# Kernel optimization log

Hardware: AMD Instinct MI355X
Metric: run time of the kernel (lower is better)

The kernel has to match this reference:

```python
import jax, jax.numpy as jnp
import numpy as np

H = 12        # num heads
DH = 64       # head dim
W = 8         # window size
WIN2 = W * W  # tokens per window


def _relative_position_index():
    # Swin-style relative position index, [WIN2, WIN2] int array (static).
    coords = np.stack(np.meshgrid(np.arange(W), np.arange(W), indexing='ij'))  # [2,W,W]
    flat = coords.reshape(2, -1)                                               # [2,WIN2]
    rel = flat[:, :, None] - flat[:, None, :]                                  # [2,WIN2,WIN2]
    rel = rel.transpose(1, 2, 0).astype(np.int64)
    rel[..., 0] += W - 1
    rel[..., 1] += W - 1
    rel[..., 0] *= 2 * W - 1
    return rel.sum(-1)  # [WIN2, WIN2]


def setup_inputs() -> dict:
    key = jax.random.key(0)
    ks = jax.random.split(key, 12)
    B, S, D = 128, 256, 768
    scale = 0.02
    return {
        'q': jax.random.normal(ks[0], (B, S, D), jnp.float32),
        'k': jax.random.normal(ks[1], (B, S, D), jnp.float32),
        'v': jax.random.normal(ks[2], (B, S, D), jnp.float32),
        'Wq': jax.random.normal(ks[3], (D, D), jnp.float32) * scale,
        'bq': jnp.zeros((D,), jnp.float32),
        'Wk': jax.random.normal(ks[4], (D, D), jnp.float32) * scale,
        'bk': jnp.zeros((D,), jnp.float32),
        'Wv': jax.random.normal(ks[5], (D, D), jnp.float32) * scale,
        'bv': jnp.zeros((D,), jnp.float32),
        'Wo': jax.random.normal(ks[6], (D, D), jnp.float32) * scale,
        'bo': jnp.zeros((D,), jnp.float32),
        'bias_table': jax.random.normal(ks[7], ((2 * W - 1) ** 2, H), jnp.float32) * scale,
    }


def reference(q, k, v, Wq, bq, Wk, bk, Wv, bv, Wo, bo, bias_table):
    B, S, D = q.shape

    def proj(x, Wt, bt):
        # Linear stores weight as [out, in]; y = x @ W^T + b, then split heads.
        return (x @ Wt.T + bt).reshape(B, S, H, DH).transpose(0, 2, 1, 3)

    qh = proj(q, Wq, bq)  # [B,H,S,DH]
    kh = proj(k, Wk, bk)
    vh = proj(v, Wv, bv)

    scores = jnp.einsum('bhqd,bhkd->bhqk', qh, kh) / np.float32(np.sqrt(DH))

    idx = _relative_position_index()                         # static [WIN2,WIN2]
    bias = bias_table[idx.reshape(-1)].reshape(WIN2, WIN2, H)
    bias = bias.transpose(2, 0, 1)                           # [H,WIN2,WIN2]
    n_contrast = S // WIN2
    bias = jnp.tile(bias, (1, n_contrast, n_contrast))       # [H,S,S]

    probs = jax.nn.softmax(scores + bias[None], axis=-1)     # dropout p=0 (eval)
    ctx = jnp.einsum('bhqk,bhkd->bhqd', probs, vh)
    ctx = ctx.transpose(0, 2, 1, 3).reshape(B, S, D)
    return ctx @ Wo.T + bo
```

## Files before the change

kernel.cpp:

```cpp
#include <hip/hip_runtime.h>


typedef __bf16 bf16;
typedef __bf16 bf16x8 __attribute__((ext_vector_type(8)));
typedef float  f32x4  __attribute__((ext_vector_type(4)));

#define MFMA_BF16(a, b, c) __builtin_amdgcn_mfma_f32_16x16x32_bf16((a), (b), (c), 0, 0, 0)

__device__ __forceinline__ void gld16(const void* g, void* l) {
    __builtin_amdgcn_global_load_lds(
        (const __attribute__((address_space(1))) void*)g,
        (__attribute__((address_space(3))) void*)l, 16, 0, 0);
}

__device__ __forceinline__ bf16x8 pack8(f32x4 lo, f32x4 hi) {
    bf16x8 r;
    r[0] = (bf16)lo[0]; r[1] = (bf16)lo[1]; r[2] = (bf16)lo[2]; r[3] = (bf16)lo[3];
    r[4] = (bf16)hi[0]; r[5] = (bf16)hi[1]; r[6] = (bf16)hi[2]; r[7] = (bf16)hi[3];
    return r;
}

__device__ __forceinline__ int swz8(int row, int g) { return g ^ (row & 7); }

__global__ __launch_bounds__(256)
void gemm_qkv(const float* __restrict__ q, const float* __restrict__ k,
              const float* __restrict__ v,
              const float* __restrict__ Wq, const float* __restrict__ Wk,
              const float* __restrict__ Wv,
              const float* __restrict__ bq, const float* __restrict__ bk,
              const float* __restrict__ bv, bf16* __restrict__ outbase)
{
    __shared__ bf16 As[128 * 64];
    __shared__ bf16 Bs[128 * 64];

    const int z = blockIdx.z;
    const float* X    = (z == 0) ? q  : (z == 1) ? k  : v;
    const float* Wt   = (z == 0) ? Wq : (z == 1) ? Wk : Wv;
    const float* bias = (z == 0) ? bq : (z == 1) ? bk : bv;
    bf16* out = outbase + (size_t)z * 25165824;

    const int tid  = threadIdx.x;
    const int m0   = blockIdx.x * 128;
    const int n0   = blockIdx.y * 128;
    const int w    = tid >> 6;
    const int lane = tid & 63;
    const int quad = lane >> 4;
    const int l15  = lane & 15;
    const int wr   = (w >> 1) * 64;
    const int wc   = (w & 1) * 64;

    f32x4 acc[4][4] = {};

    for (int kt = 0; kt < 12; ++kt) {
        const int k0 = kt * 64;
        __syncthreads();
        #pragma unroll
        for (int p = 0; p < 4; ++p) {
            int g = p * 256 + tid;
            int row = g >> 3, gp = g & 7;
            const float* src = X + (size_t)(m0 + row) * 768 + k0 + gp * 8;
            *(bf16x8*)&As[row * 64 + swz8(row, gp) * 8] =
                pack8(*(const f32x4*)src, *(const f32x4*)(src + 4));
        }
        #pragma unroll
        for (int p = 0; p < 4; ++p) {
            int g = p * 256 + tid;
            int row = g >> 3, gp = g & 7;
            const float* src = Wt + (size_t)(n0 + row) * 768 + k0 + gp * 8;
            *(bf16x8*)&Bs[row * 64 + swz8(row, gp) * 8] =
                pack8(*(const f32x4*)src, *(const f32x4*)(src + 4));
        }
        __syncthreads();
        #pragma unroll
        for (int kk = 0; kk < 2; ++kk) {
            bf16x8 af[4], bfr[4];
            #pragma unroll
            for (int mt = 0; mt < 4; ++mt) {
                int row = wr + mt * 16 + l15;
                af[mt] = *(const bf16x8*)&As[row * 64 + swz8(row, kk * 4 + quad) * 8];
            }
            #pragma unroll
            for (int nt = 0; nt < 4; ++nt) {
                int row = wc + nt * 16 + l15;
                bfr[nt] = *(const bf16x8*)&Bs[row * 64 + swz8(row, kk * 4 + quad) * 8];
            }
            #pragma unroll
            for (int mt = 0; mt < 4; ++mt)
                #pragma unroll
                for (int nt = 0; nt < 4; ++nt)
                    acc[mt][nt] = MFMA_BF16(af[mt], bfr[nt], acc[mt][nt]);
        }
    }

    #pragma unroll
    for (int mt = 0; mt < 4; ++mt) {
        #pragma unroll
        for (int nt = 0; nt < 4; ++nt) {
            int gn = n0 + wc + nt * 16 + l15;
            float bv = bias[gn];
            int h = gn >> 6, d = gn & 63;
            #pragma unroll
            for (int r = 0; r < 4; ++r) {
                int gm = m0 + wr + mt * 16 + quad * 4 + r;
                int b = gm >> 8, s = gm & 255;
                out[(((size_t)(b * 12 + h) << 8) + s) * 64 + d] = (bf16)(acc[mt][nt][r] + bv);
            }
        }
    }
}

__global__ __launch_bounds__(256)
void gemm_out(const bf16* __restrict__ X, const float* __restrict__ Wt,
              const float* __restrict__ bias, float* __restrict__ out)
{
    __shared__ bf16 As[128 * 64];
    __shared__ bf16 Bs[128 * 64];

    const int tid  = threadIdx.x;
    const int m0   = blockIdx.x * 128;
    const int n0   = blockIdx.y * 128;
    const int w    = tid >> 6;
    const int lane = tid & 63;
    const int quad = lane >> 4;
    const int l15  = lane & 15;
    const int wr   = (w >> 1) * 64;
    const int wc   = (w & 1) * 64;

    f32x4 acc[4][4] = {};

    for (int kt = 0; kt < 12; ++kt) {
        const int k0 = kt * 64;
        __syncthreads();
        #pragma unroll
        for (int p = 0; p < 4; ++p) {
            int g = p * 256 + tid;
            int row = g >> 3;
            int cg  = swz8(row, g & 7);
            gld16(X + (size_t)(m0 + row) * 768 + k0 + cg * 8,
                  (char*)As + g * 16);
        }
        #pragma unroll
        for (int p = 0; p < 4; ++p) {
            int g = p * 256 + tid;
            int row = g >> 3, gp = g & 7;
            const float* src = Wt + (size_t)(n0 + row) * 768 + k0 + gp * 8;
            *(bf16x8*)&Bs[row * 64 + swz8(row, gp) * 8] =
                pack8(*(const f32x4*)src, *(const f32x4*)(src + 4));
        }
        __syncthreads();
        #pragma unroll
        for (int kk = 0; kk < 2; ++kk) {
            bf16x8 af[4], bfr[4];
            #pragma unroll
            for (int mt = 0; mt < 4; ++mt) {
                int row = wr + mt * 16 + l15;
                af[mt] = *(const bf16x8*)&As[row * 64 + swz8(row, kk * 4 + quad) * 8];
            }
            #pragma unroll
            for (int nt = 0; nt < 4; ++nt) {
                int row = wc + nt * 16 + l15;
                bfr[nt] = *(const bf16x8*)&Bs[row * 64 + swz8(row, kk * 4 + quad) * 8];
            }
            #pragma unroll
            for (int mt = 0; mt < 4; ++mt)
                #pragma unroll
                for (int nt = 0; nt < 4; ++nt)
                    acc[mt][nt] = MFMA_BF16(af[mt], bfr[nt], acc[mt][nt]);
        }
    }

    #pragma unroll
    for (int mt = 0; mt < 4; ++mt) {
        #pragma unroll
        for (int nt = 0; nt < 4; ++nt) {
            int gn = n0 + wc + nt * 16 + l15;
            float bv = bias[gn];
            #pragma unroll
            for (int r = 0; r < 4; ++r) {
                int gm = m0 + wr + mt * 16 + quad * 4 + r;
                out[(size_t)gm * 768 + gn] = acc[mt][nt][r] + bv;
            }
        }
    }
}

__global__ __launch_bounds__(256)
void transpose_v(const bf16* __restrict__ vh, bf16* __restrict__ vt)
{
    __shared__ bf16 Ts[64 * 65];
    const int qt = blockIdx.x, h = blockIdx.y, b = blockIdx.z;
    const bf16* src = vh + ((size_t)(b * 12 + h) * 256 + qt * 64) * 64;
    bf16* dst = vt + (size_t)(b * 12 + h) * 64 * 256;

    const int tid = threadIdx.x;
    {
        int row = tid >> 2, c0 = (tid & 3) * 16;
        bf16x8 v0 = *(const bf16x8*)(src + row * 64 + c0);
        bf16x8 v1 = *(const bf16x8*)(src + row * 64 + c0 + 8);
        #pragma unroll
        for (int i = 0; i < 8; ++i) {
            Ts[row * 65 + c0 + i]     = v0[i];
            Ts[row * 65 + c0 + 8 + i] = v1[i];
        }
    }
    __syncthreads();
    {
        int d = tid >> 2, j0 = (tid & 3) * 16;
        bf16x8 o0, o1;
        #pragma unroll
        for (int i = 0; i < 8; ++i) {
            o0[i] = Ts[(j0 + i) * 65 + d];
            o1[i] = Ts[(j0 + 8 + i) * 65 + d];
        }
        *(bf16x8*)(dst + (size_t)d * 256 + qt * 64 + j0)     = o0;
        *(bf16x8*)(dst + (size_t)d * 256 + qt * 64 + j0 + 8) = o1;
    }
}

__global__ __launch_bounds__(256)
void attn_kernel(const bf16* __restrict__ qh, const bf16* __restrict__ kh,
                 const bf16* __restrict__ vt, const float* __restrict__ table,
                 bf16* __restrict__ ctx)
{
    __shared__ bf16 Qs[64 * 64];
    __shared__ bf16 Ks[64 * 64];
    __shared__ bf16 Vs[64 * 64];
    __shared__ bf16 Ps[4 * 16 * 72];
    __shared__ bf16 Bsh[64 * 68];

    const int tid  = threadIdx.x;
    const int qt   = blockIdx.x;
    const int h    = blockIdx.y;
    const int b    = blockIdx.z;
    const int w    = tid >> 6;
    const int lane = tid & 63;
    const int quad = lane >> 4;
    const int l15  = lane & 15;

    const size_t bh = (size_t)(b * 12 + h) * 256 * 64;
    const bf16* Qg  = qh + bh + (size_t)qt * 64 * 64;
    const bf16* Kg  = kh + bh;
    const bf16* Vtg = vt + bh;

    #pragma unroll
    for (int p = 0; p < 2; ++p) {
        int g = p * 256 + tid;
        gld16(Qg + (size_t)(g >> 3) * 64 + (g & 7) * 8, (char*)Qs + g * 16);
    }
    {
        int i = tid >> 2, j0 = (tid & 3) * 16;
        int ai = i >> 3, aj = i & 7;
        #pragma unroll
        for (int jj = 0; jj < 16; ++jj) {
            int j = j0 + jj;
            int idx = (ai - (j >> 3) + 7) * 15 + (aj - (j & 7) + 7);
            Bsh[i * 68 + j] = (bf16)table[idx * 12 + h];
        }
    }

    f32x4 sacc[16] = {};
    bf16x8 qf0, qf1;
    for (int c = 0; c < 4; ++c) {
        __syncthreads();
        #pragma unroll
        for (int p = 0; p < 2; ++p) {
            int g = p * 256 + tid;
            gld16(Kg + (size_t)(c * 64 + (g >> 3)) * 64 + (g & 7) * 8, (char*)Ks + g * 16);
        }
        __syncthreads();
        if (c == 0) {
            qf0 = *(const bf16x8*)&Qs[(w * 16 + l15) * 64 + quad * 8];
            qf1 = *(const bf16x8*)&Qs[(w * 16 + l15) * 64 + 32 + quad * 8];
        }
        #pragma unroll
        for (int jtl = 0; jtl < 4; ++jtl) {
            bf16x8 kf0 = *(const bf16x8*)&Ks[(jtl * 16 + l15) * 64 + quad * 8];
            bf16x8 kf1 = *(const bf16x8*)&Ks[(jtl * 16 + l15) * 64 + 32 + quad * 8];
            sacc[c * 4 + jtl] = MFMA_BF16(qf0, kf0, sacc[c * 4 + jtl]);
            sacc[c * 4 + jtl] = MFMA_BF16(qf1, kf1, sacc[c * 4 + jtl]);
        }
    }

    const int browbase = w * 16 + quad * 4;
    float p[16][4];
    #pragma unroll
    for (int jt = 0; jt < 16; ++jt) {
        int jcol = ((jt * 16) & 63) + l15;
        #pragma unroll
        for (int r = 0; r < 4; ++r)
            p[jt][r] = sacc[jt][r] * 0.125f + (float)Bsh[(browbase + r) * 68 + jcol];
    }
    float invl[4];
    #pragma unroll
    for (int r = 0; r < 4; ++r) {
        float m = p[0][r];
        #pragma unroll
        for (int jt = 1; jt < 16; ++jt) m = fmaxf(m, p[jt][r]);
        #pragma unroll
        for (int off = 1; off < 16; off <<= 1)
            m = fmaxf(m, __shfl_xor(m, off, 64));
        float s = 0.f;
        #pragma unroll
        for (int jt = 0; jt < 16; ++jt) {
            p[jt][r] = __expf(p[jt][r] - m);
            s += p[jt][r];
        }
        #pragma unroll
        for (int off = 1; off < 16; off <<= 1)
            s += __shfl_xor(s, off, 64);
        invl[r] = 1.0f / s;
    }

    f32x4 cacc[4] = {};
    bf16* Pw = &Ps[w * 16 * 72];
    for (int c = 0; c < 4; ++c) {
        __syncthreads();
        #pragma unroll
        for (int pp = 0; pp < 2; ++pp) {
            int g = pp * 256 + tid;
            gld16(Vtg + (size_t)(g >> 3) * 256 + c * 64 + (g & 7) * 8, (char*)Vs + g * 16);
        }
        #pragma unroll
        for (int jtl = 0; jtl < 4; ++jtl) {
            int jt = c * 4 + jtl;
            #pragma unroll
            for (int r = 0; r < 4; ++r)
                Pw[(quad * 4 + r) * 72 + jtl * 16 + l15] = (bf16)(p[jt][r] * invl[r]);
        }
        __syncthreads();
        bf16x8 pf0 = *(const bf16x8*)&Pw[l15 * 72 + quad * 8];
        bf16x8 pf1 = *(const bf16x8*)&Pw[l15 * 72 + 32 + quad * 8];
        #pragma unroll
        for (int dt = 0; dt < 4; ++dt) {
            bf16x8 vf0 = *(const bf16x8*)&Vs[(dt * 16 + l15) * 64 + quad * 8];
            bf16x8 vf1 = *(const bf16x8*)&Vs[(dt * 16 + l15) * 64 + 32 + quad * 8];
            cacc[dt] = MFMA_BF16(pf0, vf0, cacc[dt]);
            cacc[dt] = MFMA_BF16(pf1, vf1, cacc[dt]);
        }
    }

    const size_t obase = ((size_t)b * 256) * 768 + (size_t)h * 64;
    #pragma unroll
    for (int dt = 0; dt < 4; ++dt) {
        #pragma unroll
        for (int r = 0; r < 4; ++r) {
            int s = qt * 64 + w * 16 + quad * 4 + r;
            int d = dt * 16 + l15;
            ctx[obase + (size_t)s * 768 + d] = (bf16)cacc[dt][r];
        }
    }
}

extern "C" void kernel_launch(void* const* d_in, const int* in_sizes, int n_in,
                              void* d_out, int out_size, void* d_ws, size_t ws_size,
                              hipStream_t stream) {
    (void)in_sizes; (void)n_in; (void)out_size; (void)ws_size;
    const float* q     = (const float*)d_in[0];
    const float* k     = (const float*)d_in[1];
    const float* v     = (const float*)d_in[2];
    const float* Wq    = (const float*)d_in[3];
    const float* bq    = (const float*)d_in[4];
    const float* Wk    = (const float*)d_in[5];
    const float* bk    = (const float*)d_in[6];
    const float* Wv    = (const float*)d_in[7];
    const float* bv    = (const float*)d_in[8];
    const float* Wo    = (const float*)d_in[9];
    const float* bo    = (const float*)d_in[10];
    const float* table = (const float*)d_in[11];

    const size_t NE = (size_t)128 * 256 * 768;
    bf16* qh  = (bf16*)d_ws;
    bf16* kh  = qh + NE;
    bf16* vh  = kh + NE;
    bf16* vt  = vh + NE;
    bf16* ctx = vh;
    float* out = (float*)d_out;

    dim3 blk(256);
    gemm_qkv<<<dim3(256, 6, 3), blk, 0, stream>>>(q, k, v, Wq, Wk, Wv, bq, bk, bv, qh);
    transpose_v<<<dim3(4, 12, 128), blk, 0, stream>>>(vh, vt);
    attn_kernel<<<dim3(4, 12, 128), blk, 0, stream>>>(qh, kh, vt, table, ctx);
    gemm_out<<<dim3(256, 6), blk, 0, stream>>>(ctx, Wo, bo, out);
}
```

Measured before the change: 777.9 us.

## Double-buffer LDS tiles with register prefetch in projection GEMMs

Both the QKV projection GEMM and the output projection GEMM now use two LDS buffers. The next K-tile is loaded from global memory into registers while MFMAs run on the current tile, and one barrier per iteration replaces two. The goal is to hide global load latency behind compute. The cost is doubled shared memory (64KB per block), more registers for the prefetched fp32 data, and possibly lower occupancy. In gemm_out the direct global-to-LDS loads are replaced by ordinary register loads.

Result: faster. 739.2 us (-5.0%).

```diff
diff --git a/kernel.cpp b/kernel.cpp
--- a/kernel.cpp
+++ b/kernel.cpp
@@ -30,8 +30,8 @@
               const float* __restrict__ bq, const float* __restrict__ bk,
               const float* __restrict__ bv, bf16* __restrict__ outbase)
 {
-    __shared__ bf16 As[128 * 64];
-    __shared__ bf16 Bs[128 * 64];
+    __shared__ bf16 As[2][128 * 64];
+    __shared__ bf16 Bs[2][128 * 64];
 
     const int z = blockIdx.z;
     const float* X    = (z == 0) ? q  : (z == 1) ? k  : v;
@@ -49,40 +49,49 @@
     const int wr   = (w >> 1) * 64;
     const int wc   = (w & 1) * 64;
 
+    int srow[4], sgp[4], sdst[4];
+    #pragma unroll
+    for (int p = 0; p < 4; ++p) {
+        int g = p * 256 + tid;
+        srow[p] = g >> 3;
+        sgp[p]  = g & 7;
+        sdst[p] = srow[p] * 64 + swz8(srow[p], sgp[p]) * 8;
+    }
+
     f32x4 acc[4][4] = {};
-
-    for (int kt = 0; kt < 12; ++kt) {
-        const int k0 = kt * 64;
-        __syncthreads();
+    f32x4 aL[4], aH[4], bL[4], bH[4];
+
+    auto load_stage = [&](int k0) {
         #pragma unroll
         for (int p = 0; p < 4; ++p) {
-            int g = p * 256 + tid;
-            int row = g >> 3, gp = g & 7;
-            const float* src = X + (size_t)(m0 + row) * 768 + k0 + gp * 8;
-            *(bf16x8*)&As[row * 64 + swz8(row, gp) * 8] =
-                pack8(*(const f32x4*)src, *(const f32x4*)(src + 4));
-        }
+            const float* sa = X + (size_t)(m0 + srow[p]) * 768 + k0 + sgp[p] * 8;
+            aL[p] = *(const f32x4*)sa;
+            aH[p] = *(const f32x4*)(sa + 4);
+            const float* sb = Wt + (size_t)(n0 + srow[p]) * 768 + k0 + sgp[p] * 8;
+            bL[p] = *(const f32x4*)sb;
+            bH[p] = *(const f32x4*)(sb + 4);
+        }
+    };
+    auto write_stage = [&](int buf) {
         #pragma unroll
         for (int p = 0; p < 4; ++p) {
-            int g = p * 256 + tid;
-            int row = g >> 3, gp = g & 7;
-            const float* src = Wt + (size_t)(n0 + row) * 768 + k0 + gp * 8;
-            *(bf16x8*)&Bs[row * 64 + swz8(row, gp) * 8] =
-                pack8(*(const f32x4*)src, *(const f32x4*)(src + 4));
-        }
-        __syncthreads();
+            *(bf16x8*)&As[buf][sdst[p]] = pack8(aL[p], aH[p]);
+            *(bf16x8*)&Bs[buf][sdst[p]] = pack8(bL[p], bH[p]);
+        }
+    };
+    auto compute = [&](int buf) {
         #pragma unroll
         for (int kk = 0; kk < 2; ++kk) {
             bf16x8 af[4], bfr[4];
             #pragma unroll
             for (int mt = 0; mt < 4; ++mt) {
                 int row = wr + mt * 16 + l15;
-                af[mt] = *(const bf16x8*)&As[row * 64 + swz8(row, kk * 4 + quad) * 8];
+                af[mt] = *(const bf16x8*)&As[buf][row * 64 + swz8(row, kk * 4 + quad) * 8];
             }
             #pragma unroll
             for (int nt = 0; nt < 4; ++nt) {
                 int row = wc + nt * 16 + l15;
-                bfr[nt] = *(const bf16x8*)&Bs[row * 64 + swz8(row, kk * 4 + quad) * 8];
+                bfr[nt] = *(const bf16x8*)&Bs[buf][row * 64 + swz8(row, kk * 4 + quad) * 8];
             }
             #pragma unroll
             for (int mt = 0; mt < 4; ++mt)
@@ -90,7 +99,21 @@
                 for (int nt = 0; nt < 4; ++nt)
                     acc[mt][nt] = MFMA_BF16(af[mt], bfr[nt], acc[mt][nt]);
         }
-    }
+    };
+
+    load_stage(0);
+    write_stage(0);
+    __syncthreads();
+
+    int cur = 0;
+    for (int kt = 0; kt < 11; ++kt) {
+        load_stage((kt + 1) * 64);
+        compute(cur);
+        write_stage(cur ^ 1);
+        __syncthreads();
+        cur ^= 1;
+    }
+    compute(cur);
 
     #pragma unroll
     for (int mt = 0; mt < 4; ++mt) {
@@ -113,8 +136,8 @@
 void gemm_out(const bf16* __restrict__ X, const float* __restrict__ Wt,
               const float* __restrict__ bias, float* __restrict__ out)
 {
-    __shared__ bf16 As[128 * 64];
-    __shared__ bf16 Bs[128 * 64];
+    __shared__ bf16 As[2][128 * 64];
+    __shared__ bf16 Bs[2][128 * 64];
 
     const int tid  = threadIdx.x;
     const int m0   = blockIdx.x * 128;
@@ -126,40 +149,48 @@
     const int wr   = (w >> 1) * 64;
     const int wc   = (w & 1) * 64;
 
+    int srow[4], sgp[4], sdst[4];
+    #pragma unroll
+    for (int p = 0; p < 4; ++p) {
+        int g = p * 256 + tid;
+        srow[p] = g >> 3;
+        sgp[p]  = g & 7;
+        sdst[p] = srow[p] * 64 + swz8(srow[p], sgp[p]) * 8;
+    }
+
     f32x4 acc[4][4] = {};
-
-    for (int kt = 0; kt < 12; ++kt) {
-        const int k0 = kt * 64;
-        __syncthreads();
+    bf16x8 aR[4];
+    f32x4 bL[4], bH[4];
+
+    auto load_stage = [&](int k0) {
         #pragma unroll
         for (int p = 0; p < 4; ++p) {
-            int g = p * 256 + tid;
-            int row = g >> 3;
-            int cg  = swz8(row, g & 7);
-            gld16(X + (size_t)(m0 + row) * 768 + k0 + cg * 8,
-                  (char*)As + g * 16);
-        }
+            aR[p] = *(const bf16x8*)(X + (size_t)(m0 + srow[p]) * 768 + k0 + sgp[p] * 8);
+            const float* sb = Wt + (size_t)(n0 + srow[p]) * 768 + k0 + sgp[p] * 8;
+            bL[p] = *(const f32x4*)sb;
+            bH[p] = *(const f32x4*)(sb + 4);
+        }
+    };
+    auto write_stage = [&](int buf) {
         #pragma unroll
         for (int p = 0; p < 4; ++p) {
-            int g = p * 256 + tid;
-            int row = g >> 3, gp = g & 7;
-            const float* src = Wt + (size_t)(n0 + row) * 768 + k0 + gp * 8;
-            *(bf16x8*)&Bs[row * 64 + swz8(row, gp) * 8] =
-                pack8(*(const f32x4*)src, *(const f32x4*)(src + 4));
-        }
-        __syncthreads();
+            *(bf16x8*)&As[buf][sdst[p]] = aR[p];
+            *(bf16x8*)&Bs[buf][sdst[p]] = pack8(bL[p], bH[p]);
+        }
+    };
+    auto compute = [&](int buf) {
         #pragma unroll
         for (int kk = 0; kk < 2; ++kk) {
             bf16x8 af[4], bfr[4];
             #pragma unroll
             for (int mt = 0; mt < 4; ++mt) {
                 int row = wr + mt * 16 + l15;
-                af[mt] = *(const bf16x8*)&As[row * 64 + swz8(row, kk * 4 + quad) * 8];
+                af[mt] = *(const bf16x8*)&As[buf][row * 64 + swz8(row, kk * 4 + quad) * 8];
             }
             #pragma unroll
             for (int nt = 0; nt < 4; ++nt) {
                 int row = wc + nt * 16 + l15;
-                bfr[nt] = *(const bf16x8*)&Bs[row * 64 + swz8(row, kk * 4 + quad) * 8];
+                bfr[nt] = *(const bf16x8*)&Bs[buf][row * 64 + swz8(row, kk * 4 + quad) * 8];
             }
             #pragma unroll
             for (int mt = 0; mt < 4; ++mt)
@@ -167,7 +198,21 @@
                 for (int nt = 0; nt < 4; ++nt)
                     acc[mt][nt] = MFMA_BF16(af[mt], bfr[nt], acc[mt][nt]);
         }
-    }
+    };
+
+    load_stage(0);
+    write_stage(0);
+    __syncthreads();
+
+    int cur = 0;
+    for (int kt = 0; kt < 11; ++kt) {
+        load_stage((kt + 1) * 64);
+        compute(cur);
+        write_stage(cur ^ 1);
+        __syncthreads();
+        cur ^= 1;
+    }
+    compute(cur);
 
     #pragma unroll
     for (int mt = 0; mt < 4; ++mt) {
```
